# Kernel optimization log

Hardware: AMD Instinct MI355X
Metric: run time of the kernel (lower is better)

## Reference

```python
import jax, jax.numpy as jnp
import numpy as np

IN_F, OUT_F = 1024, 4096
RANK, K_ROT, K_SCALE = 8, 8, 8
HID = 128
ROT_GATE_BIAS, SCALE_GATE_BIAS = -4.0, -2.5
RESIDUAL_SCALE, ADAPTER_SCALE = 1.0, 1.0
CTRL_DIM = 3 * IN_F  # cls_mean_var pooling


def setup_inputs() -> dict:
    key = jax.random.key(0)
    ks = jax.random.split(key, 12)
    inp = {
        "x": jax.random.normal(ks[0], (32, 512, IN_F), jnp.float32),
        "shared_weight": 0.02 * jax.random.normal(ks[1], (OUT_F, IN_F), jnp.float32),
        "bias": jnp.zeros((OUT_F,), jnp.float32),
        "left_basis": 0.02 * jax.random.normal(ks[2], (K_ROT, IN_F, RANK), jnp.float32),
        "right_basis": 0.02 * jax.random.normal(ks[3], (K_ROT, IN_F, RANK), jnp.float32),
        "scale_basis": 0.01 * jax.random.normal(ks[4], (K_SCALE, OUT_F), jnp.float32),
        "ctrl_w1": (1.0 / np.sqrt(CTRL_DIM)) * jax.random.normal(ks[5], (HID, CTRL_DIM), jnp.float32),
        "ctrl_b1": jnp.zeros((HID,), jnp.float32),
        "rot_coeff_w": (1.0 / np.sqrt(HID)) * jax.random.normal(ks[6], (K_ROT, HID), jnp.float32),
        "rot_coeff_b": jnp.zeros((K_ROT,), jnp.float32),
        "rot_gate_w": (1.0 / np.sqrt(HID)) * jax.random.normal(ks[7], (1, HID), jnp.float32),
        "rot_gate_b": jnp.zeros((1,), jnp.float32),
        "scale_coeff_w": (1.0 / np.sqrt(HID)) * jax.random.normal(ks[8], (K_SCALE, HID), jnp.float32),
        "scale_coeff_b": jnp.zeros((K_SCALE,), jnp.float32),
        "scale_gate_w": (1.0 / np.sqrt(HID)) * jax.random.normal(ks[9], (1, HID), jnp.float32),
        "scale_gate_b": jnp.zeros((1,), jnp.float32),
    }
    return inp


def reference(x, shared_weight, bias, left_basis, right_basis, scale_basis,
              ctrl_w1, ctrl_b1, rot_coeff_w, rot_coeff_b, rot_gate_w, rot_gate_b,
              scale_coeff_w, scale_coeff_b, scale_gate_w, scale_gate_b):
    # --- controller conditioning signal: cls_mean_var pooling over tokens ---
    cls = x[:, 0]                       # [B, D]
    mean = x.mean(axis=1)               # [B, D]
    var = x.var(axis=1)                 # unbiased=False -> ddof=0
    z = jnp.concatenate([cls, mean, var], axis=-1)  # [B, 3D]

    # --- controller MLP (inferred: hidden GELU + linear heads, sigmoid gates with constant bias) ---
    h = jax.nn.gelu(z @ ctrl_w1.T + ctrl_b1)                       # [B, HID]
    rot_coeff = h @ rot_coeff_w.T + rot_coeff_b                     # [B, K_ROT]
    rot_gate = jax.nn.sigmoid(h @ rot_gate_w.T + rot_gate_b + ROT_GATE_BIAS)[:, 0]    # [B]
    scale_coeff = h @ scale_coeff_w.T + scale_coeff_b               # [B, K_SCALE]
    scale_gate = jax.nn.sigmoid(h @ scale_gate_w.T + scale_gate_b + SCALE_GATE_BIAS)[:, 0]  # [B]

    # --- skew-symmetric basis: u v^T - v u^T, Frobenius-normalized per basis ---
    basis = jnp.einsum('kdr,ker->kde', left_basis, right_basis)
    basis = basis - jnp.swapaxes(basis, -2, -1)                     # [K, D, D]
    norm = jnp.maximum(jnp.sqrt(jnp.sum(basis * basis, axis=(1, 2))), 1e-6)
    basis = basis / norm[:, None, None]

    # --- per-sample skew and Cayley rotation: (I - S/2)^{-1} (I + S/2) ---
    skew = RESIDUAL_SCALE * jnp.einsum('bk,kde->bde', rot_coeff, basis)  # [B, D, D]
    eye = jnp.eye(skew.shape[-1], dtype=skew.dtype)
    half = 0.5 * skew
    transform = jnp.linalg.solve(eye[None] - half, eye[None] + half)    # [B, D, D]

    # --- gated residual rotation of tokens ---
    rotated_x = jnp.einsum('bnd,bdh->bnh', x, transform)
    mixed_x = x + ADAPTER_SCALE * rot_gate[:, None, None] * (rotated_x - x)

    # --- shared dense + learned-scale adapter ---
    preact = mixed_x @ shared_weight.T + bias                       # [B, N, OUT_F]
    scale_delta = jnp.tanh(jnp.einsum('bk,kh->bh', scale_coeff, scale_basis))
    scale = 1.0 + ADAPTER_SCALE * scale_gate[:, None, None] * scale_delta[:, None, :]
    return preact * scale
```

## Files before the change

### kernel.cpp

```cpp
#include <hip/hip_runtime.h>
#include <hip/hip_bf16.h>

typedef unsigned short u16;
typedef short short8 __attribute__((ext_vector_type(8)));
typedef float f32x4 __attribute__((ext_vector_type(4)));

#define B_    32
#define N_    512
#define INF   1024
#define OUTF  4096
#define ROWS  16384
#define HID_  128
#define CTRL  3072

__device__ __forceinline__ u16 f2bf(float f) {
    union { float fv; unsigned int u; } v; v.fv = f;
    unsigned int x = v.u;
    unsigned int r = (x + 0x7fffu + ((x >> 16) & 1u)) >> 16;
    return (u16)r;
}

__device__ __forceinline__ void gll16(const void* g, const void* l) {
    __builtin_amdgcn_global_load_lds(
        (__attribute__((address_space(1))) void*)(unsigned long long)g,
        (__attribute__((address_space(3))) void*)(unsigned int)(unsigned long long)l,
        16, 0, 0);
}

__device__ __forceinline__ float sel16(float4 a, float4 b, float4 c4, float4 d, int m) {
    float v = a.x;
    v = (m == 1) ? a.y : v;  v = (m == 2) ? a.z : v;  v = (m == 3) ? a.w : v;
    v = (m == 4) ? b.x : v;  v = (m == 5) ? b.y : v;  v = (m == 6) ? b.z : v;  v = (m == 7) ? b.w : v;
    v = (m == 8) ? c4.x : v; v = (m == 9) ? c4.y : v; v = (m == 10) ? c4.z : v; v = (m == 11) ? c4.w : v;
    v = (m == 12) ? d.x : v; v = (m == 13) ? d.y : v; v = (m == 14) ? d.z : v; v = (m == 15) ? d.w : v;
    return v;
}

__global__ __launch_bounds__(256) void k_stats(const float* __restrict__ x,
        u16* __restrict__ xb, float* __restrict__ ps, float* __restrict__ pq) {
    int b = blockIdx.y, bn = blockIdx.x, t = threadIdx.x;
    const float4* xp = (const float4*)(x + (size_t)b*(N_*INF) + (size_t)bn*64*INF);
    size_t obase = ((size_t)b*(N_*INF) + (size_t)bn*64*INF) >> 2;
    float sx=0, sy=0, sz=0, sw=0, qx=0, qy=0, qz=0, qw=0;
    for (int n = 0; n < 64; ++n) {
        float4 v = xp[n*256 + t];
        sx += v.x; sy += v.y; sz += v.z; sw += v.w;
        qx += v.x*v.x; qy += v.y*v.y; qz += v.z*v.z; qw += v.w*v.w;
        ushort4 o; o.x = f2bf(v.x); o.y = f2bf(v.y); o.z = f2bf(v.z); o.w = f2bf(v.w);
        ((ushort4*)xb)[obase + n*256 + t] = o;
    }
    int base = (b*8 + bn)*256 + t;
    float4 s4; s4.x=sx; s4.y=sy; s4.z=sz; s4.w=sw;
    float4 q4; q4.x=qx; q4.y=qy; q4.z=qz; q4.w=qw;
    ((float4*)ps)[base] = s4;
    ((float4*)pq)[base] = q4;
}

__global__ __launch_bounds__(256) void k_ctrl(const float* __restrict__ x,
    const float* __restrict__ ps, const float* __restrict__ pq,
    const float* __restrict__ w1, const float* __restrict__ b1,
    const float* __restrict__ rcw, const float* __restrict__ rcb,
    const float* __restrict__ rgw, const float* __restrict__ rgb,
    const float* __restrict__ scw, const float* __restrict__ scb,
    const float* __restrict__ sgw, const float* __restrict__ sgb,
    float* __restrict__ rc, float* __restrict__ rg,
    float* __restrict__ sc, float* __restrict__ sg)
{
    __shared__ float zs[CTRL];
    __shared__ float hs[HID_];
    int b = blockIdx.x, t = threadIdx.x;
    for (int d = t; d < 1024; d += 256) {
        float ssum = 0.f, qsum = 0.f;
        for (int j = 0; j < 8; ++j) {
            ssum += ps[(b*8 + j)*1024 + d];
            qsum += pq[(b*8 + j)*1024 + d];
        }
        float mean = ssum * (1.0f/512.0f);
        float var  = qsum * (1.0f/512.0f) - mean*mean;
        zs[d]        = x[(size_t)b*(N_*INF) + d];
        zs[1024 + d] = mean;
        zs[2048 + d] = var;
    }
    __syncthreads();
    int w = t >> 6, l = t & 63;
    const float4* zp = (const float4*)zs;
    for (int i = w; i < HID_; i += 4) {
        const float4* wr = (const float4*)(w1 + (size_t)i*CTRL);
        float acc = 0.f;
        #pragma unroll
        for (int c = 0; c < 12; ++c) {
            float4 a4 = wr[l + 64*c];
            float4 z4 = zp[l + 64*c];
            acc += a4.x*z4.x + a4.y*z4.y + a4.z*z4.z + a4.w*z4.w;
        }
        #pragma unroll
        for (int o2 = 32; o2 > 0; o2 >>= 1) acc += __shfl_down(acc, o2, 64);
        if (l == 0) {
            float u = acc + b1[i];
            hs[i] = 0.5f*u*(1.0f + tanhf(0.7978845608028654f*(u + 0.044715f*u*u*u)));
        }
    }
    __syncthreads();
    if (t < 8) {
        float a = rcb[t]; const float* wv = rcw + t*HID_;
        for (int i = 0; i < HID_; ++i) a += hs[i]*wv[i];
        rc[b*8 + t] = a;
    } else if (t < 16) {
        int j = t - 8;
        float a = scb[j]; const float* wv = scw + j*HID_;
        for (int i = 0; i < HID_; ++i) a += hs[i]*wv[i];
        sc[b*8 + j] = a;
    } else if (t == 16) {
        float a = rgb[0] - 4.0f;
        for (int i = 0; i < HID_; ++i) a += hs[i]*rgw[i];
        rg[b] = 1.0f/(1.0f + expf(-a));
    } else if (t == 17) {
        float a = sgb[0] - 2.5f;
        for (int i = 0; i < HID_; ++i) a += hs[i]*sgw[i];
        sg[b] = 1.0f/(1.0f + expf(-a));
    }
}

__global__ __launch_bounds__(64) void k_norms(const float* __restrict__ G,
        float* __restrict__ norms) {
    int k = blockIdx.x, t = threadIdx.x;
    int i = t >> 3, j = t & 7;
    float A  = G[(16*k + i)*128     + 16*k + j];
    float C  = G[(16*k + 8 + i)*128 + 16*k + 8 + j];
    float D  = G[(16*k + 8 + i)*128 + 16*k + j];
    float Dj = G[(16*k + 8 + j)*128 + 16*k + i];
    float term = A*C - D*Dj;
    #pragma unroll
    for (int o2 = 32; o2 > 0; o2 >>= 1) term += __shfl_down(term, o2, 64);
    if (t == 0) norms[k] = fmaxf(sqrtf(fmaxf(2.0f*term, 0.0f)), 1e-6f);
}

__global__ __launch_bounds__(256) void k_buildU(const float* __restrict__ L,
        const float* __restrict__ R, float* __restrict__ U, u16* __restrict__ Utb) {
    int idx = blockIdx.x*256 + threadIdx.x;
    int d = idx >> 7, col = idx & 127;
    int k = col >> 4, rr = col & 15;
    float v = (rr < 8) ? L[((size_t)k<<13) + (d<<3) + rr]
                       : R[((size_t)k<<13) + (d<<3) + (rr-8)];
    U[idx] = v;
    Utb[col*1024 + d] = f2bf(v);
}

__global__ __launch_bounds__(256) void k_gram(const float* __restrict__ U,
        float* __restrict__ G) {
    int e = blockIdx.x*256 + threadIdx.x;
    int i = e >> 7, j = e & 127;
    float a = 0.f;
    for (int d = 0; d < 1024; ++d) a += U[d*128 + i]*U[d*128 + j];
    G[e] = a;
}

__global__ __launch_bounds__(1024, 4) void k_solve(const float* __restrict__ G,
    const float* __restrict__ rc, const float* __restrict__ norms,
    const float* __restrict__ rg, u16* __restrict__ Ptb)
{
    __shared__ float smem[16384];
    float* prow = smem;
    float* pcol = smem + 256;
    int b = blockIdx.x, t = threadIdx.x;
    int r = t & 127, s = t >> 7;
    int kr = r >> 4, rr = r & 15;
    float a_r = rc[b*8 + kr] / norms[kr];
    int partner = (rr < 8) ? (kr*16 + 8 + rr) : (kr*16 + rr - 8);
    float sg0 = (rr < 8) ? -0.5f*a_r : 0.5f*a_r;
    float4 o0, o1, o2, o3;
    {
        const float4* Gp = (const float4*)(G + (size_t)partner*128 + 16*s);
        float4 g0 = Gp[0], g1 = Gp[1], g2 = Gp[2], g3 = Gp[3];
        int base = 16*s;
        o0.x = sg0*g0.x + ((r == base+0 ) ? 1.f : 0.f);
        o0.y = sg0*g0.y + ((r == base+1 ) ? 1.f : 0.f);
        o0.z = sg0*g0.z + ((r == base+2 ) ? 1.f : 0.f);
        o0.w = sg0*g0.w + ((r == base+3 ) ? 1.f : 0.f);
        o1.x = sg0*g1.x + ((r == base+4 ) ? 1.f : 0.f);
        o1.y = sg0*g1.y + ((r == base+5 ) ? 1.f : 0.f);
        o1.z = sg0*g1.z + ((r == base+6 ) ? 1.f : 0.f);
        o1.w = sg0*g1.w + ((r == base+7 ) ? 1.f : 0.f);
        o2.x = sg0*g2.x + ((r == base+8 ) ? 1.f : 0.f);
        o2.y = sg0*g2.y + ((r == base+9 ) ? 1.f : 0.f);
        o2.z = sg0*g2.z + ((r == base+10) ? 1.f : 0.f);
        o2.w = sg0*g2.w + ((r == base+11) ? 1.f : 0.f);
        o3.x = sg0*g3.x + ((r == base+12) ? 1.f : 0.f);
        o3.y = sg0*g3.y + ((r == base+13) ? 1.f : 0.f);
        o3.z = sg0*g3.z + ((r == base+14) ? 1.f : 0.f);
        o3.w = sg0*g3.w + ((r == base+15) ? 1.f : 0.f);
    }
    if (r == 0) {
        float4 v0 = o0, v1 = o1, v2 = o2, v3 = o3;
        if (s == 0) v0.x += 1.0f;
        *(float4*)(prow + 16*s +  0) = v0;
        *(float4*)(prow + 16*s +  4) = v1;
        *(float4*)(prow + 16*s +  8) = v2;
        *(float4*)(prow + 16*s + 12) = v3;
    }
    if (s == 0) pcol[r] = o0.x;
    __syncthreads();
    for (int c = 0; c < 128; ++c) {
        int buf = c & 1, nb = buf ^ 1;
        float fr = pcol[buf*128 + r];
        const float4* prp = (const float4*)(prow + buf*128 + 16*s);
        float4 p0 = prp[0], p1 = prp[1], p2 = prp[2], p3 = prp[3];
        float pv = prow[buf*128 + c] - 1.0f;
        float invp = 1.0f / pv;
        if (r == c) {
            int base = 16*s;
            o0.x = (base+0  == c) ? invp : o0.x*invp;
            o0.y = (base+1  == c) ? invp : o0.y*invp;
            o0.z = (base+2  == c) ? invp : o0.z*invp;
            o0.w = (base+3  == c) ? invp : o0.w*invp;
            o1.x = (base+4  == c) ? invp : o1.x*invp;
            o1.y = (base+5  == c) ? invp : o1.y*invp;
            o1.z = (base+6  == c) ? invp : o1.z*invp;
            o1.w = (base+7  == c) ? invp : o1.w*invp;
            o2.x = (base+8  == c) ? invp : o2.x*invp;
            o2.y = (base+9  == c) ? invp : o2.y*invp;
            o2.z = (base+10 == c) ? invp : o2.z*invp;
            o2.w = (base+11 == c) ? invp : o2.w*invp;
            o3.x = (base+12 == c) ? invp : o3.x*invp;
            o3.y = (base+13 == c) ? invp : o3.y*invp;
            o3.z = (base+14 == c) ? invp : o3.z*invp;
            o3.w = (base+15 == c) ? invp : o3.w*invp;
        } else {
            float fi = fr * invp;
            o0.x -= fi*p0.x; o0.y -= fi*p0.y; o0.z -= fi*p0.z; o0.w -= fi*p0.w;
            o1.x -= fi*p1.x; o1.y -= fi*p1.y; o1.z -= fi*p1.z; o1.w -= fi*p1.w;
            o2.x -= fi*p2.x; o2.y -= fi*p2.y; o2.z -= fi*p2.z; o2.w -= fi*p2.w;
            o3.x -= fi*p3.x; o3.y -= fi*p3.y; o3.z -= fi*p3.z; o3.w -= fi*p3.w;
        }
        int cn = c + 1;
        if (cn < 128) {
            if (r == cn) {
                float4 v0 = o0, v1 = o1, v2 = o2, v3 = o3;
                int base = 16*s;
                v0.x += (base+0  == cn) ? 1.f : 0.f;
                v0.y += (base+1  == cn) ? 1.f : 0.f;
                v0.z += (base+2  == cn) ? 1.f : 0.f;
                v0.w += (base+3  == cn) ? 1.f : 0.f;
                v1.x += (base+4  == cn) ? 1.f : 0.f;
                v1.y += (base+5  == cn) ? 1.f : 0.f;
                v1.z += (base+6  == cn) ? 1.f : 0.f;
                v1.w += (base+7  == cn) ? 1.f : 0.f;
                v2.x += (base+8  == cn) ? 1.f : 0.f;
                v2.y += (base+9  == cn) ? 1.f : 0.f;
                v2.z += (base+10 == cn) ? 1.f : 0.f;
                v2.w += (base+11 == cn) ? 1.f : 0.f;
                v3.x += (base+12 == cn) ? 1.f : 0.f;
                v3.y += (base+13 == cn) ? 1.f : 0.f;
                v3.z += (base+14 == cn) ? 1.f : 0.f;
                v3.w += (base+15 == cn) ? 1.f : 0.f;
                *(float4*)(prow + nb*128 + 16*s +  0) = v0;
                *(float4*)(prow + nb*128 + 16*s +  4) = v1;
                *(float4*)(prow + nb*128 + 16*s +  8) = v2;
                *(float4*)(prow + nb*128 + 16*s + 12) = v3;
            }
            if (s == (cn >> 4)) pcol[nb*128 + r] = sel16(o0, o1, o2, o3, cn & 15);
        }
        __syncthreads();
    }
    float as_ = rc[b*8 + s] / norms[s];
    float gg = rg[b];
    float na = -gg * as_, pa = gg * as_;
    smem[(16*s +  0)*128 + r] = na*o2.x;
    smem[(16*s +  1)*128 + r] = na*o2.y;
    smem[(16*s +  2)*128 + r] = na*o2.z;
    smem[(16*s +  3)*128 + r] = na*o2.w;
    smem[(16*s +  4)*128 + r] = na*o3.x;
    smem[(16*s +  5)*128 + r] = na*o3.y;
    smem[(16*s +  6)*128 + r] = na*o3.z;
    smem[(16*s +  7)*128 + r] = na*o3.w;
    smem[(16*s +  8)*128 + r] = pa*o0.x;
    smem[(16*s +  9)*128 + r] = pa*o0.y;
    smem[(16*s + 10)*128 + r] = pa*o0.z;
    smem[(16*s + 11)*128 + r] = pa*o0.w;
    smem[(16*s + 12)*128 + r] = pa*o1.x;
    smem[(16*s + 13)*128 + r] = pa*o1.y;
    smem[(16*s + 14)*128 + r] = pa*o1.z;
    smem[(16*s + 15)*128 + r] = pa*o1.w;
    __syncthreads();
    int r2 = t >> 3, s2 = t & 7;
    const float4* rp = (const float4*)(smem + r2*128 + 16*s2);
    float4 v0 = rp[0], v1 = rp[1], v2 = rp[2], v3 = rp[3];
    uint4 w0, w1;
    w0.x = f2bf(v0.x) | ((unsigned)f2bf(v0.y) << 16);
    w0.y = f2bf(v0.z) | ((unsigned)f2bf(v0.w) << 16);
    w0.z = f2bf(v1.x) | ((unsigned)f2bf(v1.y) << 16);
    w0.w = f2bf(v1.z) | ((unsigned)f2bf(v1.w) << 16);
    w1.x = f2bf(v2.x) | ((unsigned)f2bf(v2.y) << 16);
    w1.y = f2bf(v2.z) | ((unsigned)f2bf(v2.w) << 16);
    w1.z = f2bf(v3.x) | ((unsigned)f2bf(v3.y) << 16);
    w1.w = f2bf(v3.z) | ((unsigned)f2bf(v3.w) << 16);
    uint4* dst = (uint4*)(Ptb + ((size_t)(b*128 + r2))*128 + 16*s2);
    dst[0] = w0; dst[1] = w1;
}

__global__ __launch_bounds__(256) void k_scale(const float* __restrict__ sc,
    const float* __restrict__ sbasis, const float* __restrict__ sg,
    float* __restrict__ scl) {
    int idx = blockIdx.x*256 + threadIdx.x;
    int b = idx >> 12, o = idx & 4095;
    float a = 0.f;
    #pragma unroll
    for (int k = 0; k < 8; ++k) a += sc[b*8 + k]*sbasis[(k<<12) + o];
    scl[idx] = 1.0f + sg[b]*tanhf(a);
}

__global__ __launch_bounds__(256) void k_cvt(const float* __restrict__ in,
        u16* __restrict__ out, int n4) {
    int i = blockIdx.x*256 + threadIdx.x;
    if (i < n4) {
        float4 v = ((const float4*)in)[i];
        ushort4 o; o.x=f2bf(v.x); o.y=f2bf(v.y); o.z=f2bf(v.z); o.w=f2bf(v.w);
        ((ushort4*)out)[i] = o;
    }
}

__global__ __launch_bounds__(256) void k_gemm_bt(const u16* __restrict__ A,
    const u16* __restrict__ Bt, u16* __restrict__ C,
    int M, int N, int K, long sA_, long sB_, long sC_)
{
    A  += (size_t)blockIdx.z * sA_;
    Bt += (size_t)blockIdx.z * sB_;
    C  += (size_t)blockIdx.z * sC_;
    int bm = blockIdx.y, bn = blockIdx.x;
    __shared__ __align__(16) u16 sA[128*64];
    __shared__ __align__(16) u16 sB[128*64];
    int tid = threadIdx.x;
    int wave = tid >> 6, lane = tid & 63;
    int wbase = tid & ~63;
    int wm = wave >> 1, wn = wave & 1;
    int quad = lane >> 4, l16 = lane & 15;
    f32x4 acc[4][4];
    #pragma unroll
    for (int i = 0; i < 4; ++i)
        #pragma unroll
        for (int j = 0; j < 4; ++j) { f32x4 z4 = {0.f,0.f,0.f,0.f}; acc[i][j] = z4; }
    int nk = K >> 6;
    for (int kt = 0; kt < nk; ++kt) {
        __syncthreads();
        #pragma unroll
        for (int q2 = 0; q2 < 4; ++q2) {
            int c = q2*256 + tid, row = c >> 3, kc = c & 7;
            gll16(A  + (size_t)(bm*128 + row)*K + kt*64 + kc*8, sA + (size_t)(q2*256 + wbase)*8);
            gll16(Bt + (size_t)(bn*128 + row)*K + kt*64 + kc*8, sB + (size_t)(q2*256 + wbase)*8);
        }
        __syncthreads();
        #pragma unroll
        for (int ks = 0; ks < 2; ++ks) {
            short8 af[4], bfv[4];
            #pragma unroll
            for (int i = 0; i < 4; ++i)
                af[i] = *(const short8*)(sA + (wm*64 + i*16 + l16)*64 + ks*32 + quad*8);
            #pragma unroll
            for (int j = 0; j < 4; ++j)
                bfv[j] = *(const short8*)(sB + (wn*64 + j*16 + l16)*64 + ks*32 + quad*8);
            #pragma unroll
            for (int i = 0; i < 4; ++i)
                #pragma unroll
                for (int j = 0; j < 4; ++j)
                    acc[i][j] = __builtin_amdgcn_mfma_f32_16x16x32_bf16(af[i], bfv[j], acc[i][j], 0, 0, 0);
        }
    }
    #pragma unroll
    for (int i = 0; i < 4; ++i)
        #pragma unroll
        for (int j = 0; j < 4; ++j) {
            int gcol = bn*128 + wn*64 + j*16 + l16;
            #pragma unroll
            for (int r = 0; r < 4; ++r) {
                int grow = bm*128 + wm*64 + i*16 + quad*4 + r;
                C[(size_t)grow*N + gcol] = f2bf(acc[i][j][r]);
            }
        }
}

__global__ __launch_bounds__(256) void k_main(const u16* __restrict__ xb,
    const u16* __restrict__ Wb, const u16* __restrict__ Qb,
    const u16* __restrict__ Vb, const float* __restrict__ bias,
    const float* __restrict__ scale, float* __restrict__ out)
{
    int flat = blockIdx.y * 32 + blockIdx.x;
    int wg   = (flat & 7) * 512 + (flat >> 3);
    int bm = wg >> 5, bn = wg & 31;
    __shared__ __align__(16) u16 sA[128*64];
    __shared__ __align__(16) u16 sB[128*64];
    int tid = threadIdx.x;
    int wave = tid >> 6, lane = tid & 63;
    int wbase = tid & ~63;
    int wm = wave >> 1, wn = wave & 1;
    int quad = lane >> 4, l16 = lane & 15;
    f32x4 acc[4][4];
    #pragma unroll
    for (int i = 0; i < 4; ++i)
        #pragma unroll
        for (int j = 0; j < 4; ++j) { f32x4 z4 = {0.f,0.f,0.f,0.f}; acc[i][j] = z4; }
    for (int kt = 0; kt < 18; ++kt) {
        __syncthreads();
        if (kt < 16) {
            #pragma unroll
            for (int q2 = 0; q2 < 4; ++q2) {
                int c = q2*256 + tid, row = c >> 3, kc = c & 7;
                gll16(xb + (size_t)(bm*128 + row)*1024 + kt*64 + kc*8, sA + (size_t)(q2*256 + wbase)*8);
                gll16(Wb + (size_t)(bn*128 + row)*1024 + kt*64 + kc*8, sB + (size_t)(q2*256 + wbase)*8);
            }
        } else {
            int k0 = (kt - 16)*64;
            #pragma unroll
            for (int q2 = 0; q2 < 4; ++q2) {
                int c = q2*256 + tid, row = c >> 3, kc = c & 7;
                gll16(Qb + (size_t)(bm*128 + row)*128 + k0 + kc*8, sA + (size_t)(q2*256 + wbase)*8);
                gll16(Vb + (size_t)(bn*128 + row)*128 + k0 + kc*8, sB + (size_t)(q2*256 + wbase)*8);
            }
        }
        __syncthreads();
        #pragma unroll
        for (int ks = 0; ks < 2; ++ks) {
            short8 af[4], bfv[4];
            #pragma unroll
            for (int i = 0; i < 4; ++i)
                af[i] = *(const short8*)(sA + (wm*64 + i*16 + l16)*64 + ks*32 + quad*8);
            #pragma unroll
            for (int j = 0; j < 4; ++j)
                bfv[j] = *(const short8*)(sB + (wn*64 + j*16 + l16)*64 + ks*32 + quad*8);
            #pragma unroll
            for (int i = 0; i < 4; ++i)
                #pragma unroll
                for (int j = 0; j < 4; ++j)
                    acc[i][j] = __builtin_amdgcn_mfma_f32_16x16x32_bf16(af[i], bfv[j], acc[i][j], 0, 0, 0);
        }
    }
    const float* scrow = scale + (bm >> 2)*4096;
    #pragma unroll
    for (int i = 0; i < 4; ++i)
        #pragma unroll
        for (int j = 0; j < 4; ++j) {
            int gcol = bn*128 + wn*64 + j*16 + l16;
            float bc = bias[gcol];
            float sv = scrow[gcol];
            #pragma unroll
            for (int r = 0; r < 4; ++r) {
                int grow = bm*128 + wm*64 + i*16 + quad*4 + r;
                out[(size_t)grow*4096 + gcol] = (acc[i][j][r] + bc) * sv;
            }
        }
}

extern "C" void kernel_launch(void* const* d_in, const int* in_sizes, int n_in,
                              void* d_out, int out_size, void* d_ws, size_t ws_size,
                              hipStream_t stream)
{
    const float* x     = (const float*)d_in[0];
    const float* Wsh   = (const float*)d_in[1];
    const float* bias  = (const float*)d_in[2];
    const float* left  = (const float*)d_in[3];
    const float* right = (const float*)d_in[4];
    const float* sbasis= (const float*)d_in[5];
    const float* w1    = (const float*)d_in[6];
    const float* b1    = (const float*)d_in[7];
    const float* rcw   = (const float*)d_in[8];
    const float* rcb   = (const float*)d_in[9];
    const float* rgw   = (const float*)d_in[10];
    const float* rgb   = (const float*)d_in[11];
    const float* scw   = (const float*)d_in[12];
    const float* scb   = (const float*)d_in[13];
    const float* sgw   = (const float*)d_in[14];
    const float* sgb   = (const float*)d_in[15];
    float* out = (float*)d_out;
    (void)in_sizes; (void)n_in; (void)out_size; (void)ws_size;

    char* wsp = (char*)d_ws;
    size_t off = 0;
    auto take = [&](size_t bytes) -> char* {
        char* p = wsp + off;
        off = (off + bytes + 255) & ~(size_t)255;
        return p;
    };
    u16*   xb   = (u16*)  take((size_t)ROWS*INF*2);
    u16*   Wb   = (u16*)  take((size_t)OUTF*INF*2);
    u16*   Utb  = (u16*)  take((size_t)128*1024*2);
    u16*   Yb   = (u16*)  take((size_t)ROWS*128*2);
    u16*   Qb   = (u16*)  take((size_t)ROWS*128*2);
    u16*   Vb   = (u16*)  take((size_t)OUTF*128*2);
    u16*   Ptb  = (u16*)  take((size_t)32*128*128*2);
    float* Uf   = (float*)take((size_t)1024*128*4);
    float* Gf   = (float*)take((size_t)128*128*4);
    float* ps   = (float*)take((size_t)32*8*1024*4);
    float* pq   = (float*)take((size_t)32*8*1024*4);
    float* rc   = (float*)take(32*8*4);
    float* sc   = (float*)take(32*8*4);
    float* rg   = (float*)take(32*4);
    float* sg   = (float*)take(32*4);
    float* nrm  = (float*)take(8*4);
    float* scl  = (float*)take((size_t)32*4096*4);

    k_cvt   <<<dim3(4096),   dim3(256), 0, stream>>>(Wsh, Wb, OUTF*INF/4);
    k_stats <<<dim3(8,32),   dim3(256), 0, stream>>>(x, xb, ps, pq);
    k_buildU<<<dim3(512),    dim3(256), 0, stream>>>(left, right, Uf, Utb);
    k_gram  <<<dim3(64),     dim3(256), 0, stream>>>(Uf, Gf);
    k_norms <<<dim3(8),      dim3(64),  0, stream>>>(Gf, nrm);
    k_ctrl  <<<dim3(32),     dim3(256), 0, stream>>>(x, ps, pq, w1, b1, rcw, rcb,
                                                     rgw, rgb, scw, scb, sgw, sgb,
                                                     rc, rg, sc, sg);
    k_solve <<<dim3(32),     dim3(1024), 0, stream>>>(Gf, rc, nrm, rg, Ptb);
    k_scale <<<dim3(512),    dim3(256), 0, stream>>>(sc, sbasis, sg, scl);
    k_gemm_bt<<<dim3(1,128,1), dim3(256), 0, stream>>>(xb, Utb, Yb, ROWS, 128, 1024, 0L, 0L, 0L);
    k_gemm_bt<<<dim3(1,4,32),  dim3(256), 0, stream>>>(Yb, Ptb, Qb, 512, 128, 128,
                                                       (long)512*128, (long)128*128, (long)512*128);
    k_gemm_bt<<<dim3(1,32,1),  dim3(256), 0, stream>>>(Wb, Utb, Vb, OUTF, 128, 1024, 0L, 0L, 0L);
    k_main  <<<dim3(32,128), dim3(256), 0, stream>>>(xb, Wb, Qb, Vb, bias, scl, out);
}
```

Before: 847.2 us.

## Restructure main GEMM into 256x256 tiles with double-buffered swizzled LDS pipeline

The main fused GEMM goes from 128x128 tiles with 4 waves to 256x256 tiles with 8 waves. Global-to-LDS loads are double-buffered so the next K-tile loads while MFMAs run on the current one, and the LDS layout is XOR-swizzled to avoid bank conflicts. This targets load latency stalls, the two barriers per K step and global traffic per output element. In exchange it uses 128 KB of LDS and 128 accumulator registers per lane, so occupancy is lower and the grid has only 1024 blocks.

```diff
diff --git a/kernel.cpp b/kernel.cpp
--- a/kernel.cpp
+++ b/kernel.cpp
@@ -378,75 +378,102 @@
         }
 }
 
-__global__ __launch_bounds__(256) void k_main(const u16* __restrict__ xb,
+__global__ __launch_bounds__(512, 2) void k_main(const u16* __restrict__ xb,
     const u16* __restrict__ Wb, const u16* __restrict__ Qb,
     const u16* __restrict__ Vb, const float* __restrict__ bias,
     const float* __restrict__ scale, float* __restrict__ out)
 {
-    int flat = blockIdx.y * 32 + blockIdx.x;
-    int wg   = (flat & 7) * 512 + (flat >> 3);
-    int bm = wg >> 5, bn = wg & 31;
-    __shared__ __align__(16) u16 sA[128*64];
-    __shared__ __align__(16) u16 sB[128*64];
+    __shared__ __align__(16) u16 lds[65536];
+    int flat = blockIdx.y * 16 + blockIdx.x;
+    int wg   = (flat & 7) * 128 + (flat >> 3);
+    int bm = wg >> 4, bn = wg & 15;
     int tid = threadIdx.x;
     int wave = tid >> 6, lane = tid & 63;
-    int wbase = tid & ~63;
-    int wm = wave >> 1, wn = wave & 1;
+    int wm = wave >> 2, wn = wave & 3;
     int quad = lane >> 4, l16 = lane & 15;
-    f32x4 acc[4][4];
+
+    int srow = wave*16 + (lane >> 3);
+    int scol = (((lane & 7) ^ ((lane >> 3) & 7)) << 3);
+    int arow0 = bm*256 + srow;
+    int brow0 = bn*256 + srow;
+
+    int cswz0 = (quad*16)      ^ ((l16 & 7) << 4);
+    int cswz1 = (64 + quad*16) ^ ((l16 & 7) << 4);
+    int abase = wm*16384 + l16*128;
+    int bbase = 32768 + (wn >> 1)*16384 + (wn & 1)*8192 + l16*128;
+
+    auto stageg = [&](int kt, int bf) {
+        u16* lb = lds + bf*32768;
+        const u16 *As, *Bs; int str, ko;
+        if (kt < 16) { As = xb; Bs = Wb; str = 1024; ko = kt*64 + scol; }
+        else         { As = Qb; Bs = Vb; str = 128;  ko = (kt-16)*64 + scol; }
+        #pragma unroll
+        for (int i = 0; i < 2; ++i) {
+            int r = i*8;
+            gll16(As + (size_t)(arow0 + r)*str + ko,       lb +         wave*1024 + i*512);
+            gll16(As + (size_t)(arow0 + 128 + r)*str + ko, lb +  8192 + wave*1024 + i*512);
+            gll16(Bs + (size_t)(brow0 + r)*str + ko,       lb + 16384 + wave*1024 + i*512);
+            gll16(Bs + (size_t)(brow0 + 128 + r)*str + ko, lb + 24576 + wave*1024 + i*512);
+        }
+    };
+
+    f32x4 acc[8][4];
     #pragma unroll
-    for (int i = 0; i < 4; ++i)
-        #pragma unroll
-        for (int j = 0; j < 4; ++j) { f32x4 z4 = {0.f,0.f,0.f,0.f}; acc[i][j] = z4; }
-    for (int kt = 0; kt < 18; ++kt) {
-        __syncthreads();
-        if (kt < 16) {
-            #pragma unroll
-            for (int q2 = 0; q2 < 4; ++q2) {
-                int c = q2*256 + tid, row = c >> 3, kc = c & 7;
-                gll16(xb + (size_t)(bm*128 + row)*1024 + kt*64 + kc*8, sA + (size_t)(q2*256 + wbase)*8);
-                gll16(Wb + (size_t)(bn*128 + row)*1024 + kt*64 + kc*8, sB + (size_t)(q2*256 + wbase)*8);
+    for (int m = 0; m < 8; ++m)
+        #pragma unroll
+        for (int n = 0; n < 4; ++n) { f32x4 z4 = {0.f,0.f,0.f,0.f}; acc[m][n] = z4; }
+
+    stageg(0, 0);
+    stageg(1, 1);
+    asm volatile("s_waitcnt vmcnt(8)" ::: "memory");
+    __builtin_amdgcn_s_barrier();
+    __builtin_amdgcn_sched_barrier(0);
+
+    for (int it = 0; it < 9; ++it) {
+        #pragma unroll
+        for (int hf = 0; hf < 2; ++hf) {
+            const char* lb = (const char*)lds + hf*65536;
+            short8 bfr[4][2];
+            #pragma unroll
+            for (int n = 0; n < 4; ++n) {
+                bfr[n][0] = *(const short8*)(lb + bbase + cswz0 + n*2048);
+                bfr[n][1] = *(const short8*)(lb + bbase + cswz1 + n*2048);
             }
-        } else {
-            int k0 = (kt - 16)*64;
-            #pragma unroll
-            for (int q2 = 0; q2 < 4; ++q2) {
-                int c = q2*256 + tid, row = c >> 3, kc = c & 7;
-                gll16(Qb + (size_t)(bm*128 + row)*128 + k0 + kc*8, sA + (size_t)(q2*256 + wbase)*8);
-                gll16(Vb + (size_t)(bn*128 + row)*128 + k0 + kc*8, sB + (size_t)(q2*256 + wbase)*8);
+            if (hf == 0) { if (it >= 1) stageg(2*it + 1, 1); }
+            else         { if (it <= 7) stageg(2*it + 2, 0); }
+            __builtin_amdgcn_s_setprio(1);
+            #pragma unroll
+            for (int m = 0; m < 8; ++m) {
+                short8 a0 = *(const short8*)(lb + abase + cswz0 + m*2048);
+                short8 a1 = *(const short8*)(lb + abase + cswz1 + m*2048);
+                #pragma unroll
+                for (int n = 0; n < 4; ++n) {
+                    acc[m][n] = __builtin_amdgcn_mfma_f32_16x16x32_bf16(a0, bfr[n][0], acc[m][n], 0, 0, 0);
+                    acc[m][n] = __builtin_amdgcn_mfma_f32_16x16x32_bf16(a1, bfr[n][1], acc[m][n], 0, 0, 0);
+                }
             }
-        }
-        __syncthreads();
-        #pragma unroll
-        for (int ks = 0; ks < 2; ++ks) {
-            short8 af[4], bfv[4];
-            #pragma unroll
-            for (int i = 0; i < 4; ++i)
-                af[i] = *(const short8*)(sA + (wm*64 + i*16 + l16)*64 + ks*32 + quad*8);
-            #pragma unroll
-            for (int j = 0; j < 4; ++j)
-                bfv[j] = *(const short8*)(sB + (wn*64 + j*16 + l16)*64 + ks*32 + quad*8);
-            #pragma unroll
-            for (int i = 0; i < 4; ++i)
-                #pragma unroll
-                for (int j = 0; j < 4; ++j)
-                    acc[i][j] = __builtin_amdgcn_mfma_f32_16x16x32_bf16(af[i], bfv[j], acc[i][j], 0, 0, 0);
-        }
-    }
-    const float* scrow = scale + (bm >> 2)*4096;
+            __builtin_amdgcn_s_setprio(0);
+            __builtin_amdgcn_sched_barrier(0);
+            asm volatile("s_waitcnt vmcnt(0)" ::: "memory");
+            __builtin_amdgcn_s_barrier();
+            __builtin_amdgcn_sched_barrier(0);
+        }
+    }
+
+    const float* scrow = scale + (bm >> 1)*4096;
     #pragma unroll
-    for (int i = 0; i < 4; ++i)
-        #pragma unroll
-        for (int j = 0; j < 4; ++j) {
-            int gcol = bn*128 + wn*64 + j*16 + l16;
-            float bc = bias[gcol];
-            float sv = scrow[gcol];
-            #pragma unroll
-            for (int r = 0; r < 4; ++r) {
-                int grow = bm*128 + wm*64 + i*16 + quad*4 + r;
-                out[(size_t)grow*4096 + gcol] = (acc[i][j][r] + bc) * sv;
-            }
-        }
+    for (int n = 0; n < 4; ++n) {
+        int gcol = bn*256 + wn*64 + n*16 + l16;
+        float bc = bias[gcol];
+        float sv = scrow[gcol];
+        #pragma unroll
+        for (int m = 0; m < 8; ++m) {
+            int growb = bm*256 + wm*128 + m*16 + quad*4;
+            #pragma unroll
+            for (int r = 0; r < 4; ++r)
+                out[(size_t)(growb + r)*4096 + gcol] = (acc[m][n][r] + bc) * sv;
+        }
+    }
 }
 
 extern "C" void kernel_launch(void* const* d_in, const int* in_sizes, int n_in,
@@ -511,5 +538,5 @@
     k_gemm_bt<<<dim3(1,4,32),  dim3(256), 0, stream>>>(Yb, Ptb, Qb, 512, 128, 128,
                                                        (long)512*128, (long)128*128, (long)512*128);
     k_gemm_bt<<<dim3(1,32,1),  dim3(256), 0, stream>>>(Wb, Utb, Vb, OUTF, 128, 1024, 0L, 0L, 0L);
-    k_main  <<<dim3(32,128), dim3(256), 0, stream>>>(xb, Wb, Qb, Vb, bias, scl, out);
-}
+    k_main  <<<dim3(16,64), dim3(512), 0, stream>>>(xb, Wb, Qb, Vb, bias, scl, out);
+}
```

Result: faster. 784.9 us (-7.4%).
